# Kernel optimization log

Hardware: AMD Instinct MI355X
Metric: run time of the kernel (lower is better)

The kernel has to match this reference:

```python
import jax, jax.numpy as jnp
import numpy as np

# Winograd F(4x4, 3x3) transform matrices (wincnn convention, as in jiecaoyu/winograd)
BT = jnp.array([
    [4.,  0., -5.,  0., 1., 0.],
    [0., -4., -4.,  1., 1., 0.],
    [0.,  4., -4., -1., 1., 0.],
    [0., -2., -1.,  2., 1., 0.],
    [0.,  2., -1., -2., 1., 0.],
    [0.,  4.,  0., -5., 0., 1.]], dtype=jnp.float32)  # [6,6]
AT = jnp.array([
    [1., 1.,  1., 1.,  1., 0.],
    [0., 1., -1., 2., -2., 0.],
    [0., 1.,  1., 4.,  4., 0.],
    [0., 1., -1., 8., -8., 1.]], dtype=jnp.float32)  # [4,6]

KERNEL = 3
PAD = 1
GROUPS = 1
TILE_IN = 6   # input_tile_size
TILE_OUT = 4  # output_tile_size


def setup_inputs() -> dict:
    key = jax.random.key(0)
    k1, k2, k3 = jax.random.split(key, 3)
    N, Cin, H, W = 16, 64, 128, 128
    Cout = 64
    x = jax.random.normal(k1, (N, Cin, H, W), dtype=jnp.float32)
    # weight is stored in the Winograd (6x6 spectral) domain, as in the module
    weight = jax.random.normal(k2, (Cout, Cin // GROUPS, TILE_IN, TILE_IN), dtype=jnp.float32) * 0.01
    bias = jax.random.normal(k3, (Cout,), dtype=jnp.float32) * 0.01
    return {"x": x, "weight": weight, "bias": bias}


def reference(x, weight, bias):
    N, Cin, H0, W0 = x.shape
    Cout = weight.shape[0]
    g = GROUPS
    # conv padding
    x = jnp.pad(x, ((0, 0), (0, 0), (PAD, PAD), (PAD, PAD)))
    H = x.shape[2]
    out_w = H - KERNEL + 1
    # pad so output width is a multiple of the output tile size
    extra = (-out_w) % TILE_OUT
    if extra:
        x = jnp.pad(x, ((0, 0), (0, 0), (0, extra), (0, extra)))
    nt = (x.shape[2] - TILE_IN) // TILE_OUT + 1  # tiles per spatial dim
    # extract overlapping 6x6 tiles with stride 4 (the torch unfold)
    idx = jnp.arange(nt)[:, None] * TILE_OUT + jnp.arange(TILE_IN)[None, :]  # [nt,6]
    tiles = x[:, :, idx]                 # [N,C,nt,6,Wp]
    tiles = tiles[:, :, :, :, idx]       # [N,C,nt,6,nt,6]
    # input transform: V = BT @ d @ BT^T per tile -> [N,C,nt,nt,6,6]
    V = jnp.einsum('ai,ncpiqj,bj->ncpqab', BT, tiles, BT)
    # grouped spectral GEMM over input channels
    Vg = V.reshape(N, g, Cin // g, nt, nt, TILE_IN, TILE_IN)
    Wg = weight.reshape(g, Cout // g, Cin // g, TILE_IN, TILE_IN)
    M = jnp.einsum('goiab,ngipqab->ngopqab', Wg, Vg)
    M = M.reshape(N, Cout, nt, nt, TILE_IN, TILE_IN)
    # output transform: Y = AT @ M @ AT^T per tile -> [N,O,nt,nt,4,4]
    Y = jnp.einsum('xa,nopqab,yb->nopqxy', AT, M, AT)
    # stitch tiles back: [N,O,nt,4,nt,4] -> [N,O,nt*4,nt*4]
    y = Y.transpose(0, 1, 2, 4, 3, 5).reshape(N, Cout, nt * TILE_OUT, nt * TILE_OUT)
    y = y + bias[None, :, None, None]
    # crop the extra padding
    y = y[:, :, :out_w, :out_w]
    return y
```

## Files before the change

kernel.cpp:

```cpp
#include <hip/hip_runtime.h>
#include <stdint.h>

typedef __attribute__((ext_vector_type(4))) float f32x4;
typedef __attribute__((ext_vector_type(8))) short s16x8;

#define WB_BYTES 294912

__device__ __forceinline__ short f2bf(float f) {
    uint32_t u = __builtin_bit_cast(uint32_t, f);
    u = u + 0x7FFFu + ((u >> 16) & 1u);
    return (short)(u >> 16);
}

__global__ __launch_bounds__(256) void wtrans(const float* __restrict__ wf, short* __restrict__ wb) {
    int tid = blockIdx.x * 256 + threadIdx.x;
    const float* src = wf + tid * 36;
    float w[36];
#pragma unroll
    for (int i = 0; i < 9; i++) {
        f32x4 v = *(const f32x4*)(src + 4 * i);
        w[4*i+0] = v[0]; w[4*i+1] = v[1]; w[4*i+2] = v[2]; w[4*i+3] = v[3];
    }
#pragma unroll
    for (int ab = 0; ab < 36; ab++) wb[ab * 4096 + tid] = f2bf(w[ab]);
}

#define XS 343
__global__ __launch_bounds__(512, 2) void wino_fused(const float* __restrict__ x,
                                                     const short* __restrict__ wb,
                                                     const float* __restrict__ bias,
                                                     float* __restrict__ out) {
    __shared__ __align__(16) float SM[20192];
    float* X = SM;
    short* Vs = (short*)(SM + 32 * XS);
    float* P = SM;

    int t = threadIdx.x;
    int lane = t & 63;
    int w = t >> 6;
    int cog = w >> 1;
    int sh = w & 1;
    int lo = lane & 15;
    int kq = lane >> 4;

    int b = blockIdx.x;
    int n = b >> 6;
    int sb = b & 63;
    int p0 = (sb >> 3) * 4;
    int q0 = (sb & 7) * 4;
    const float* xb = x + (size_t)n * 64 * 16384;
    int row0 = 4 * p0 - 1;
    int col0a = 4 * q0 - 4;

    int tl = t >> 5;
    int ci = t & 31;
    int tp = tl >> 2, tq = tl & 3;

    f32x4 acc[18];
#pragma unroll
    for (int i = 0; i < 18; i++) acc[i] = (f32x4){0.f, 0.f, 0.f, 0.f};

#pragma unroll
    for (int r = 0; r < 2; r++) {
#pragma unroll
        for (int i = 0; i < 7; i++) {
            int s = i * 512 + t;
            if (s < 3456) {
                int cis = s / 108;
                int rs = s - cis * 108;
                int row = rs / 6;
                int c4 = rs - row * 6;
                int gr = row0 + row;
                int gc = col0a + 4 * c4;
                float v0 = 0.f, v1 = 0.f, v2 = 0.f, v3 = 0.f;
                if ((unsigned)gr < 128u) {
                    const float* rowp = xb + (size_t)((r * 32 + cis) * 128 + gr) * 128;
                    if (gc >= 0 && gc + 3 < 128) {
                        f32x4 v = *(const f32x4*)(rowp + gc);
                        v0 = v[0]; v1 = v[1]; v2 = v[2]; v3 = v[3];
                    } else {
                        if ((unsigned)(gc + 0) < 128u) v0 = rowp[gc + 0];
                        if ((unsigned)(gc + 1) < 128u) v1 = rowp[gc + 1];
                        if ((unsigned)(gc + 2) < 128u) v2 = rowp[gc + 2];
                        if ((unsigned)(gc + 3) < 128u) v3 = rowp[gc + 3];
                    }
                }
                int base = cis * XS + row * 18;
                int cl = 4 * c4 - 3;
                if ((unsigned)(cl + 0) < 18u) X[base + cl + 0] = v0;
                if ((unsigned)(cl + 1) < 18u) X[base + cl + 1] = v1;
                if ((unsigned)(cl + 2) < 18u) X[base + cl + 2] = v2;
                if ((unsigned)(cl + 3) < 18u) X[base + cl + 3] = v3;
            }
        }
        __syncthreads();

        {
            const float* Xb = X + ci * XS + (4 * tp) * 18 + 4 * tq;
            short* vb = Vs + tl * 32 + ci;
#pragma unroll
            for (int s2 = 0; s2 < 2; s2++) {
                float Ua[3][6];
#pragma unroll
                for (int c = 0; c < 6; c++) {
                    float m0 = Xb[0 * 18 + c], m1 = Xb[1 * 18 + c], m2 = Xb[2 * 18 + c];
                    float m3 = Xb[3 * 18 + c], m4 = Xb[4 * 18 + c], m5 = Xb[5 * 18 + c];
                    if (s2 == 0) {
                        float e = fmaf(-4.f, m2, m4);
                        float f = fmaf(-4.f, m1, m3);
                        Ua[0][c] = fmaf(4.f, m0 - m2, m4 - m2);
                        Ua[1][c] = e + f;
                        Ua[2][c] = e - f;
                    } else {
                        float g = m4 - m2, h = m3 - m1;
                        Ua[0][c] = fmaf(2.f, h, g);
                        Ua[1][c] = fmaf(-2.f, h, g);
                        Ua[2][c] = fmaf(4.f, m1 - m3, m5 - m3);
                    }
                }
#pragma unroll
                for (int ar = 0; ar < 3; ar++) {
                    float m0 = Ua[ar][0], m1 = Ua[ar][1], m2 = Ua[ar][2];
                    float m3 = Ua[ar][3], m4 = Ua[ar][4], m5 = Ua[ar][5];
                    float e = fmaf(-4.f, m2, m4);
                    float f = fmaf(-4.f, m1, m3);
                    float g = m4 - m2;
                    float h = m3 - m1;
                    int abb = (s2 * 3 + ar) * 6;
                    vb[(abb + 0) * 512] = f2bf(fmaf(4.f, m0 - m2, g));
                    vb[(abb + 1) * 512] = f2bf(e + f);
                    vb[(abb + 2) * 512] = f2bf(e - f);
                    vb[(abb + 3) * 512] = f2bf(fmaf(2.f, h, g));
                    vb[(abb + 4) * 512] = f2bf(fmaf(-2.f, h, g));
                    vb[(abb + 5) * 512] = f2bf(fmaf(4.f, m1 - m3, m5 - m3));
                }
            }
        }
        __syncthreads();

        {
            const short* wb_base = wb + (sh * 18) * 4096 + (cog * 16 + lo) * 64 + r * 32 + kq * 8;
            const short* v_base = Vs + (sh * 18) * 512 + lo * 32 + kq * 8;
#pragma unroll
            for (int abl = 0; abl < 18; abl++) {
                s16x8 a0 = *(const s16x8*)(wb_base + abl * 4096);
                s16x8 b0 = *(const s16x8*)(v_base + abl * 512);
                acc[abl] = __builtin_amdgcn_mfma_f32_16x16x32_bf16(a0, b0, acc[abl], 0, 0, 0);
            }
        }
    }

    __syncthreads();
    int p = p0 + (lo >> 2);
    int q = q0 + (lo & 3);

    if (sh == 1) {
#pragma unroll
        for (int rr = 0; rr < 4; rr++) {
            float z[4][6];
#pragma unroll
            for (int bb = 0; bb < 6; bb++) {
                float m3 = acc[bb][rr], m4 = acc[6 + bb][rr], m5 = acc[12 + bb][rr];
                float sv = m3 + m4, dv = m3 - m4;
                z[0][bb] = sv;
                z[1][bb] = 2.f * dv;
                z[2][bb] = 4.f * sv;
                z[3][bb] = fmaf(8.f, dv, m5);
            }
#pragma unroll
            for (int xr = 0; xr < 4; xr++) {
                float s1 = z[xr][1] + z[xr][2], d1 = z[xr][1] - z[xr][2];
                float s2 = z[xr][3] + z[xr][4], d2 = z[xr][3] - z[xr][4];
                f32x4 y;
                y[0] = z[xr][0] + s1 + s2;
                y[1] = fmaf(2.f, d2, d1);
                y[2] = fmaf(4.f, s2, s1);
                y[3] = fmaf(8.f, d2, d1) + z[xr][5];
                *(f32x4*)&P[cog * 4096 + (rr * 4 + xr) * 256 + lane * 4] = y;
            }
        }
    }
    __syncthreads();
    if (sh == 0) {
#pragma unroll
        for (int rr = 0; rr < 4; rr++) {
            int co = cog * 16 + kq * 4 + rr;
            float bv = bias[co];
            float z[4][6];
#pragma unroll
            for (int bb = 0; bb < 6; bb++) {
                float m0 = acc[bb][rr], m1 = acc[6 + bb][rr], m2 = acc[12 + bb][rr];
                float s1 = m1 + m2, d1 = m1 - m2;
                z[0][bb] = m0 + s1;
                z[1][bb] = d1;
                z[2][bb] = s1;
                z[3][bb] = d1;
            }
            float* ob = out + ((size_t)(n * 64 + co) * 128 + 4 * p) * 128 + 4 * q;
#pragma unroll
            for (int xr = 0; xr < 4; xr++) {
                float s1 = z[xr][1] + z[xr][2], d1 = z[xr][1] - z[xr][2];
                float s2 = z[xr][3] + z[xr][4], d2 = z[xr][3] - z[xr][4];
                f32x4 part = *(const f32x4*)&P[cog * 4096 + (rr * 4 + xr) * 256 + lane * 4];
                f32x4 y;
                y[0] = z[xr][0] + s1 + s2 + part[0] + bv;
                y[1] = fmaf(2.f, d2, d1) + part[1] + bv;
                y[2] = fmaf(4.f, s2, s1) + part[2] + bv;
                y[3] = fmaf(8.f, d2, d1) + z[xr][5] + part[3] + bv;
                *(f32x4*)(ob + xr * 128) = y;
            }
        }
    }
}

extern "C" void kernel_launch(void* const* d_in, const int* in_sizes, int n_in,
                              void* d_out, int out_size, void* d_ws, size_t ws_size,
                              hipStream_t stream) {
    const float* x    = (const float*)d_in[0];
    const float* wf   = (const float*)d_in[1];
    const float* bias = (const float*)d_in[2];
    float* out = (float*)d_out;

    if (ws_size < WB_BYTES) return;
    short* wb = (short*)d_ws;

    wtrans<<<16, 256, 0, stream>>>(wf, wb);
    wino_fused<<<1024, 512, 0, stream>>>(x, wb, bias, out);
}
```

Measured before the change: 191.4 us.

## Split Winograd work across 1024-thread blocks with 2x2 spectral quadrant waves

Doubles the block to 1024 threads. Each wave now owns a 3x3 quadrant of the 6x6 spectral domain instead of 18 frequencies, so the accumulators drop from 18 to 9 per thread. The input transform is split across threads by row half, and the output transform is reduced through two 64KB shared-memory partial buffers with an extra barrier stage. This trades fewer registers per thread and more parallelism for larger LDS use (128KB), which limits each CU to one block, plus more synchronization.

```diff
diff --git a/kernel.cpp b/kernel.cpp
--- a/kernel.cpp
+++ b/kernel.cpp
@@ -26,45 +26,49 @@
 }
 
 #define XS 343
-__global__ __launch_bounds__(512, 2) void wino_fused(const float* __restrict__ x,
-                                                     const short* __restrict__ wb,
-                                                     const float* __restrict__ bias,
-                                                     float* __restrict__ out) {
-    __shared__ __align__(16) float SM[20192];
+__global__ __launch_bounds__(1024) void wino_fused(const float* __restrict__ x,
+                                                   const short* __restrict__ wb,
+                                                   const float* __restrict__ bias,
+                                                   float* __restrict__ out) {
+    __shared__ __align__(16) float SM[32768];
     float* X = SM;
     short* Vs = (short*)(SM + 32 * XS);
-    float* P = SM;
+    float* P0 = SM;
+    float* P1 = SM + 16384;
 
     int t = threadIdx.x;
     int lane = t & 63;
     int w = t >> 6;
-    int cog = w >> 1;
-    int sh = w & 1;
+    int cog = w >> 2;
+    int grp = w & 3;
+    int sh = grp >> 1;
+    int bh = grp & 1;
     int lo = lane & 15;
     int kq = lane >> 4;
 
     int b = blockIdx.x;
     int n = b >> 6;
     int sb = b & 63;
-    int p0 = (sb >> 3) * 4;
-    int q0 = (sb & 7) * 4;
+    int p0_ = (sb >> 3) * 4;
+    int q0_ = (sb & 7) * 4;
     const float* xb = x + (size_t)n * 64 * 16384;
-    int row0 = 4 * p0 - 1;
-    int col0a = 4 * q0 - 4;
-
-    int tl = t >> 5;
-    int ci = t & 31;
-    int tp = tl >> 2, tq = tl & 3;
-
-    f32x4 acc[18];
-#pragma unroll
-    for (int i = 0; i < 18; i++) acc[i] = (f32x4){0.f, 0.f, 0.f, 0.f};
+    int row0 = 4 * p0_ - 1;
+    int col0a = 4 * q0_ - 4;
+
+    int ci_t = t & 31;
+    int tl_t = (t >> 5) & 15;
+    int s2_t = t >> 9;
+    int tp = tl_t >> 2, tq = tl_t & 3;
+
+    f32x4 acc[9];
+#pragma unroll
+    for (int i = 0; i < 9; i++) acc[i] = (f32x4){0.f, 0.f, 0.f, 0.f};
 
 #pragma unroll
     for (int r = 0; r < 2; r++) {
 #pragma unroll
-        for (int i = 0; i < 7; i++) {
-            int s = i * 512 + t;
+        for (int i = 0; i < 4; i++) {
+            int s = i * 1024 + t;
             if (s < 3456) {
                 int cis = s / 108;
                 int rs = s - cis * 108;
@@ -96,119 +100,139 @@
         __syncthreads();
 
         {
-            const float* Xb = X + ci * XS + (4 * tp) * 18 + 4 * tq;
-            short* vb = Vs + tl * 32 + ci;
-#pragma unroll
-            for (int s2 = 0; s2 < 2; s2++) {
-                float Ua[3][6];
-#pragma unroll
-                for (int c = 0; c < 6; c++) {
+            const float* Xb = X + ci_t * XS + (4 * tp) * 18 + 4 * tq;
+            float Ua[3][6];
+#pragma unroll
+            for (int c = 0; c < 6; c++) {
+                if (s2_t == 0) {
                     float m0 = Xb[0 * 18 + c], m1 = Xb[1 * 18 + c], m2 = Xb[2 * 18 + c];
-                    float m3 = Xb[3 * 18 + c], m4 = Xb[4 * 18 + c], m5 = Xb[5 * 18 + c];
-                    if (s2 == 0) {
-                        float e = fmaf(-4.f, m2, m4);
-                        float f = fmaf(-4.f, m1, m3);
-                        Ua[0][c] = fmaf(4.f, m0 - m2, m4 - m2);
-                        Ua[1][c] = e + f;
-                        Ua[2][c] = e - f;
-                    } else {
-                        float g = m4 - m2, h = m3 - m1;
-                        Ua[0][c] = fmaf(2.f, h, g);
-                        Ua[1][c] = fmaf(-2.f, h, g);
-                        Ua[2][c] = fmaf(4.f, m1 - m3, m5 - m3);
-                    }
-                }
-#pragma unroll
-                for (int ar = 0; ar < 3; ar++) {
-                    float m0 = Ua[ar][0], m1 = Ua[ar][1], m2 = Ua[ar][2];
-                    float m3 = Ua[ar][3], m4 = Ua[ar][4], m5 = Ua[ar][5];
+                    float m3 = Xb[3 * 18 + c], m4 = Xb[4 * 18 + c];
                     float e = fmaf(-4.f, m2, m4);
                     float f = fmaf(-4.f, m1, m3);
-                    float g = m4 - m2;
-                    float h = m3 - m1;
-                    int abb = (s2 * 3 + ar) * 6;
-                    vb[(abb + 0) * 512] = f2bf(fmaf(4.f, m0 - m2, g));
-                    vb[(abb + 1) * 512] = f2bf(e + f);
-                    vb[(abb + 2) * 512] = f2bf(e - f);
-                    vb[(abb + 3) * 512] = f2bf(fmaf(2.f, h, g));
-                    vb[(abb + 4) * 512] = f2bf(fmaf(-2.f, h, g));
-                    vb[(abb + 5) * 512] = f2bf(fmaf(4.f, m1 - m3, m5 - m3));
-                }
+                    Ua[0][c] = fmaf(4.f, m0 - m2, m4 - m2);
+                    Ua[1][c] = e + f;
+                    Ua[2][c] = e - f;
+                } else {
+                    float m1 = Xb[1 * 18 + c], m2 = Xb[2 * 18 + c];
+                    float m3 = Xb[3 * 18 + c], m4 = Xb[4 * 18 + c], m5 = Xb[5 * 18 + c];
+                    float g = m4 - m2, h = m3 - m1;
+                    Ua[0][c] = fmaf(2.f, h, g);
+                    Ua[1][c] = fmaf(-2.f, h, g);
+                    Ua[2][c] = fmaf(4.f, m1 - m3, m5 - m3);
+                }
+            }
+            short* vb = Vs + tl_t * 32 + ci_t;
+#pragma unroll
+            for (int ar = 0; ar < 3; ar++) {
+                float m0 = Ua[ar][0], m1 = Ua[ar][1], m2 = Ua[ar][2];
+                float m3 = Ua[ar][3], m4 = Ua[ar][4], m5 = Ua[ar][5];
+                float e = fmaf(-4.f, m2, m4);
+                float f = fmaf(-4.f, m1, m3);
+                float g = m4 - m2;
+                float h = m3 - m1;
+                int abb = (s2_t * 3 + ar) * 6;
+                vb[(abb + 0) * 512] = f2bf(fmaf(4.f, m0 - m2, g));
+                vb[(abb + 1) * 512] = f2bf(e + f);
+                vb[(abb + 2) * 512] = f2bf(e - f);
+                vb[(abb + 3) * 512] = f2bf(fmaf(2.f, h, g));
+                vb[(abb + 4) * 512] = f2bf(fmaf(-2.f, h, g));
+                vb[(abb + 5) * 512] = f2bf(fmaf(4.f, m1 - m3, m5 - m3));
             }
         }
         __syncthreads();
 
         {
-            const short* wb_base = wb + (sh * 18) * 4096 + (cog * 16 + lo) * 64 + r * 32 + kq * 8;
-            const short* v_base = Vs + (sh * 18) * 512 + lo * 32 + kq * 8;
-#pragma unroll
-            for (int abl = 0; abl < 18; abl++) {
-                s16x8 a0 = *(const s16x8*)(wb_base + abl * 4096);
-                s16x8 b0 = *(const s16x8*)(v_base + abl * 512);
-                acc[abl] = __builtin_amdgcn_mfma_f32_16x16x32_bf16(a0, b0, acc[abl], 0, 0, 0);
+            const short* wb_base = wb + (cog * 16 + lo) * 64 + r * 32 + kq * 8;
+            const short* v_base = Vs + lo * 32 + kq * 8;
+#pragma unroll
+            for (int ar = 0; ar < 3; ar++) {
+#pragma unroll
+                for (int br = 0; br < 3; br++) {
+                    int ab = (3 * sh + ar) * 6 + (3 * bh + br);
+                    s16x8 a0 = *(const s16x8*)(wb_base + ab * 4096);
+                    s16x8 b0 = *(const s16x8*)(v_base + ab * 512);
+                    acc[ar * 3 + br] = __builtin_amdgcn_mfma_f32_16x16x32_bf16(a0, b0, acc[ar * 3 + br], 0, 0, 0);
+                }
             }
         }
     }
 
     __syncthreads();
-    int p = p0 + (lo >> 2);
-    int q = q0 + (lo & 3);
-
-    if (sh == 1) {
+    int p = p0_ + (lo >> 2);
+    int q = q0_ + (lo & 3);
+    float* Pown = (sh == 0) ? P0 : P1;
+
+    if (bh == 0) {
 #pragma unroll
         for (int rr = 0; rr < 4; rr++) {
-            float z[4][6];
-#pragma unroll
-            for (int bb = 0; bb < 6; bb++) {
-                float m3 = acc[bb][rr], m4 = acc[6 + bb][rr], m5 = acc[12 + bb][rr];
-                float sv = m3 + m4, dv = m3 - m4;
-                z[0][bb] = sv;
-                z[1][bb] = 2.f * dv;
-                z[2][bb] = 4.f * sv;
-                z[3][bb] = fmaf(8.f, dv, m5);
+            float z[4][3];
+#pragma unroll
+            for (int br = 0; br < 3; br++) {
+                float ma = acc[br][rr], mb = acc[3 + br][rr], mc = acc[6 + br][rr];
+                if (sh == 0) {
+                    float s1 = mb + mc, d1 = mb - mc;
+                    z[0][br] = ma + s1; z[1][br] = d1; z[2][br] = s1; z[3][br] = d1;
+                } else {
+                    float sv = ma + mb, dv = ma - mb;
+                    z[0][br] = sv; z[1][br] = 2.f * dv; z[2][br] = 4.f * sv;
+                    z[3][br] = fmaf(8.f, dv, mc);
+                }
             }
 #pragma unroll
             for (int xr = 0; xr < 4; xr++) {
                 float s1 = z[xr][1] + z[xr][2], d1 = z[xr][1] - z[xr][2];
-                float s2 = z[xr][3] + z[xr][4], d2 = z[xr][3] - z[xr][4];
                 f32x4 y;
-                y[0] = z[xr][0] + s1 + s2;
-                y[1] = fmaf(2.f, d2, d1);
-                y[2] = fmaf(4.f, s2, s1);
-                y[3] = fmaf(8.f, d2, d1) + z[xr][5];
-                *(f32x4*)&P[cog * 4096 + (rr * 4 + xr) * 256 + lane * 4] = y;
+                y[0] = z[xr][0] + s1; y[1] = d1; y[2] = s1; y[3] = d1;
+                *(f32x4*)&Pown[cog * 4096 + (rr * 4 + xr) * 256 + lane * 4] = y;
             }
         }
     }
     __syncthreads();
-    if (sh == 0) {
+    if (bh == 1) {
 #pragma unroll
         for (int rr = 0; rr < 4; rr++) {
-            int co = cog * 16 + kq * 4 + rr;
-            float bv = bias[co];
-            float z[4][6];
-#pragma unroll
-            for (int bb = 0; bb < 6; bb++) {
-                float m0 = acc[bb][rr], m1 = acc[6 + bb][rr], m2 = acc[12 + bb][rr];
-                float s1 = m1 + m2, d1 = m1 - m2;
-                z[0][bb] = m0 + s1;
-                z[1][bb] = d1;
-                z[2][bb] = s1;
-                z[3][bb] = d1;
-            }
-            float* ob = out + ((size_t)(n * 64 + co) * 128 + 4 * p) * 128 + 4 * q;
+            float z[4][3];
+#pragma unroll
+            for (int br = 0; br < 3; br++) {
+                float ma = acc[br][rr], mb = acc[3 + br][rr], mc = acc[6 + br][rr];
+                if (sh == 0) {
+                    float s1 = mb + mc, d1 = mb - mc;
+                    z[0][br] = ma + s1; z[1][br] = d1; z[2][br] = s1; z[3][br] = d1;
+                } else {
+                    float sv = ma + mb, dv = ma - mb;
+                    z[0][br] = sv; z[1][br] = 2.f * dv; z[2][br] = 4.f * sv;
+                    z[3][br] = fmaf(8.f, dv, mc);
+                }
+            }
 #pragma unroll
             for (int xr = 0; xr < 4; xr++) {
-                float s1 = z[xr][1] + z[xr][2], d1 = z[xr][1] - z[xr][2];
-                float s2 = z[xr][3] + z[xr][4], d2 = z[xr][3] - z[xr][4];
-                f32x4 part = *(const f32x4*)&P[cog * 4096 + (rr * 4 + xr) * 256 + lane * 4];
+                float s2 = z[xr][0] + z[xr][1], d2 = z[xr][0] - z[xr][1];
                 f32x4 y;
-                y[0] = z[xr][0] + s1 + s2 + part[0] + bv;
-                y[1] = fmaf(2.f, d2, d1) + part[1] + bv;
-                y[2] = fmaf(4.f, s2, s1) + part[2] + bv;
-                y[3] = fmaf(8.f, d2, d1) + z[xr][5] + part[3] + bv;
-                *(f32x4*)(ob + xr * 128) = y;
-            }
+                y[0] = s2; y[1] = 2.f * d2; y[2] = 4.f * s2;
+                y[3] = fmaf(8.f, d2, z[xr][2]);
+                float* pp = &Pown[cog * 4096 + (rr * 4 + xr) * 256 + lane * 4];
+                f32x4 old = *(const f32x4*)pp;
+                *(f32x4*)pp = old + y;
+            }
+        }
+    }
+    __syncthreads();
+    {
+        int rr = grp;
+        int co = cog * 16 + kq * 4 + rr;
+        float bv = bias[co];
+        float* ob = out + ((size_t)(n * 64 + co) * 128 + 4 * p) * 128 + 4 * q;
+#pragma unroll
+        for (int xr = 0; xr < 4; xr++) {
+            int idx = cog * 4096 + (rr * 4 + xr) * 256 + lane * 4;
+            f32x4 a0 = *(const f32x4*)&P0[idx];
+            f32x4 a1 = *(const f32x4*)&P1[idx];
+            f32x4 y;
+            y[0] = a0[0] + a1[0] + bv;
+            y[1] = a0[1] + a1[1] + bv;
+            y[2] = a0[2] + a1[2] + bv;
+            y[3] = a0[3] + a1[3] + bv;
+            *(f32x4*)(ob + xr * 128) = y;
         }
     }
 }
@@ -225,5 +249,5 @@
     short* wb = (short*)d_ws;
 
     wtrans<<<16, 256, 0, stream>>>(wf, wb);
-    wino_fused<<<1024, 512, 0, stream>>>(x, wb, bias, out);
-}
+    wino_fused<<<1024, 1024, 0, stream>>>(x, wb, bias, out);
+}
```

Result: faster. 185.9 us (-2.9%).
